# Kernel optimization log

Hardware: AMD Instinct MI355X
Metric: run time of the kernel (lower is better)

Reference implementation:

```python
import jax, jax.numpy as jnp
import numpy as np

N_NODES = 50000
N_EDGES = 800000
IN_CH = 128
HIDDEN = 32
HEADS = 4
NEG_SLOPE = 0.2


def segment_softmax(e, seg, num_segments):
    # numerically stable softmax over edges grouped by destination node
    m = jax.ops.segment_max(e, seg, num_segments=num_segments)
    ex = jnp.exp(e - m[seg])
    denom = jax.ops.segment_sum(ex, seg, num_segments=num_segments)
    return ex / denom[seg]


def gat_layer(x, src, dst, W, a_src, a_dst, b, num_nodes, concat):
    H, C = a_src.shape
    h = (x @ W).reshape(num_nodes, H, C)            # (N, H, C)
    alpha_s = jnp.einsum('nhc,hc->nh', h, a_src)    # (N, H)
    alpha_d = jnp.einsum('nhc,hc->nh', h, a_dst)    # (N, H)
    e = jax.nn.leaky_relu(alpha_s[src] + alpha_d[dst], negative_slope=NEG_SLOPE)  # (E, H)
    att = segment_softmax(e, dst, num_nodes)        # (E, H)
    out = jax.ops.segment_sum(h[src] * att[:, :, None], dst, num_segments=num_nodes)  # (N, H, C)
    if concat:
        out = out.reshape(num_nodes, H * C)
    else:
        out = out.mean(axis=1)
    return out + b


def setup_inputs() -> dict:
    key = jax.random.key(0)
    ks = jax.random.split(key, 12)
    s = 0.1
    return {
        'x': jax.random.normal(ks[0], (N_NODES, IN_CH), dtype=jnp.float32),
        'edge_index': jax.random.randint(ks[1], (2, N_EDGES), 0, N_NODES, dtype=jnp.int64),
        'W1': jax.random.normal(ks[2], (IN_CH, HEADS * HIDDEN), dtype=jnp.float32) * s,
        'a_src1': jax.random.normal(ks[3], (HEADS, HIDDEN), dtype=jnp.float32) * s,
        'a_dst1': jax.random.normal(ks[4], (HEADS, HIDDEN), dtype=jnp.float32) * s,
        'b1': jnp.zeros((HEADS * HIDDEN,), dtype=jnp.float32),
        'W2': jax.random.normal(ks[5], (HEADS * HIDDEN, 1 * HIDDEN), dtype=jnp.float32) * s,
        'a_src2': jax.random.normal(ks[6], (1, HIDDEN), dtype=jnp.float32) * s,
        'a_dst2': jax.random.normal(ks[7], (1, HIDDEN), dtype=jnp.float32) * s,
        'b2': jnp.zeros((HIDDEN,), dtype=jnp.float32),
    }


def reference(x, edge_index, W1, a_src1, a_dst1, b1, W2, a_src2, a_dst2, b2):
    n = x.shape[0]
    loops = jnp.arange(n, dtype=edge_index.dtype)
    src = jnp.concatenate([edge_index[0], loops])  # PyG GATConv add_self_loops=True
    dst = jnp.concatenate([edge_index[1], loops])
    h = gat_layer(x, src, dst, W1, a_src1, a_dst1, b1, n, concat=True)
    h = jax.nn.elu(h)  # ELU between layers (dropout=0.0)
    out = gat_layer(h, src, dst, W2, a_src2, a_dst2, b2, n, concat=False)
    return out
```

## Files before the change

kernel.cpp:

```cpp
#include <hip/hip_runtime.h>
#include <cstdint>

#define NEG_SLOPE 0.2f
#define LDA 136
#define HB  256
#define CAP 5120
#define SMEM_BYTES (64 * LDA * 2)

__device__ __forceinline__ float leaky(float v) { return v > 0.f ? v : NEG_SLOPE * v; }
__device__ __forceinline__ float elu(float v) { return v > 0.f ? v : __expf(v) - 1.f; }

typedef _Float16 half2v __attribute__((ext_vector_type(2)));
typedef _Float16 f16x8 __attribute__((ext_vector_type(8)));
typedef float f32x4 __attribute__((ext_vector_type(4)));
union H8 { float4 f4; half2v h[4]; f16x8 v8; };
union H4 { float2 f2; half2v h[2]; };
union HF2 { float2 f2; _Float16 h[4]; };
union HH { f16x8 v; half2v h[4]; };


__device__ __forceinline__ void prep_body(int bid, int G, int tid,
        const float* __restrict__ W1, const float* __restrict__ W2,
        _Float16* __restrict__ W1t, _Float16* __restrict__ W2t) {
    for (int i = bid * 256 + tid; i < 128 * 128; i += G * 256) {
        int c = i >> 7, k = i & 127;
        W1t[i] = (_Float16)W1[k * 128 + c];
    }
    for (int i = bid * 256 + tid; i < 32 * 128; i += G * 256) {
        int c = i >> 7, k = i & 127;
        W2t[i] = (_Float16)W2[k * 32 + c];
    }
}

__device__ __forceinline__ void hist_chunk(int c, int tid, int* lh,
        const int* __restrict__ dstp, int* __restrict__ hist, int E, int NB, int CH) {
    for (int t = tid; t < NB; t += 256) lh[t] = 0;
    __syncthreads();
    int e0 = c * CH, e1 = min(e0 + CH, E);
    int nv = (e1 - e0) & ~3;
    for (int i = e0 + tid * 4; i < e0 + nv; i += 1024) {
        int4 d = *(const int4*)(dstp + i);
        atomicAdd(&lh[d.x >> 8], 1);
        atomicAdd(&lh[d.y >> 8], 1);
        atomicAdd(&lh[d.z >> 8], 1);
        atomicAdd(&lh[d.w >> 8], 1);
    }
    for (int i = e0 + nv + tid; i < e1; i += 256)
        atomicAdd(&lh[dstp[i] >> 8], 1);
    __syncthreads();
    for (int t = tid; t < NB; t += 256) hist[t * HB + c] = lh[t];
}

__device__ __forceinline__ void pair_chunk(int c, int tid, int* lcur,
        const int* __restrict__ src, const int* __restrict__ dstp,
        const int* __restrict__ hist, int2* __restrict__ pairs,
        int E, int NB, int CH) {
    for (int b = tid; b < NB; b += 256) {
        const int4* row = (const int4*)(hist + b * HB);
        int s = 0;
        int c4 = c >> 2;
#pragma unroll 4
        for (int i = 0; i < c4; ++i) { int4 v = row[i]; s += v.x + v.y + v.z + v.w; }
        for (int i = c4 * 4; i < c; ++i) s += hist[b * HB + i];
        lcur[b] = s;
    }
    __syncthreads();
    int e0 = c * CH, e1 = min(e0 + CH, E);
    int nv = (e1 - e0) & ~3;
    for (int i = e0 + tid * 4; i < e0 + nv; i += 1024) {
        int4 d = *(const int4*)(dstp + i);
        int4 s = *(const int4*)(src + i);
        int b0 = d.x >> 8, b1 = d.y >> 8, b2 = d.z >> 8, b3 = d.w >> 8;
        int r0 = atomicAdd(&lcur[b0], 1);
        int r1 = atomicAdd(&lcur[b1], 1);
        int r2 = atomicAdd(&lcur[b2], 1);
        int r3 = atomicAdd(&lcur[b3], 1);
        if (r0 < CAP) pairs[(size_t)b0 * CAP + r0] = make_int2(s.x, d.x & 255);
        if (r1 < CAP) pairs[(size_t)b1 * CAP + r1] = make_int2(s.y, d.y & 255);
        if (r2 < CAP) pairs[(size_t)b2 * CAP + r2] = make_int2(s.z, d.z & 255);
        if (r3 < CAP) pairs[(size_t)b3 * CAP + r3] = make_int2(s.w, d.w & 255);
    }
    for (int i = e0 + nv + tid; i < e1; i += 256) {
        int d = dstp[i];
        int b = d >> 8;
        int r = atomicAdd(&lcur[b], 1);
        if (r < CAP) pairs[(size_t)b * CAP + r] = make_int2(src[i], d & 255);
    }
}

__device__ __forceinline__ void gemm1_tile(int b, int tid, _Float16* Ah,
        const float* __restrict__ x, const _Float16* __restrict__ W1t,
        const float* __restrict__ a_src, const float* __restrict__ a_dst,
        _Float16* __restrict__ h1h, float* __restrict__ as1, float* __restrict__ ad1,
        int n) {
    int row0 = b * 64;
    const float4* x4 = (const float4*)x;
#pragma unroll
    for (int i = 0; i < 8; ++i) {
        int idx = tid + i * 256;
        int row = idx >> 5, c4 = idx & 31;
        float4 v = make_float4(0.f, 0.f, 0.f, 0.f);
        if (row0 + row < n) v = x4[(size_t)(row0 + row) * 32 + c4];
        HF2 u;
        u.h[0] = (_Float16)v.x; u.h[1] = (_Float16)v.y;
        u.h[2] = (_Float16)v.z; u.h[3] = (_Float16)v.w;
        *(float2*)&Ah[row * LDA + c4 * 4] = u.f2;
    }
    __syncthreads();

    int l = tid & 63, w = tid >> 6;
    int lr = l & 15, lg = l >> 4;
    f16x8 af[4];
#pragma unroll
    for (int kk = 0; kk < 4; ++kk)
        af[kk] = *(const f16x8*)&Ah[(w * 16 + lr) * LDA + kk * 32 + lg * 8];
    f32x4 acc[8];
#pragma unroll
    for (int t = 0; t < 8; ++t) acc[t] = (f32x4)0.f;
#pragma unroll
    for (int t = 0; t < 8; ++t) {
#pragma unroll
        for (int kk = 0; kk < 4; ++kk) {
            f16x8 bf = *(const f16x8*)&W1t[(size_t)(t * 16 + lr) * 128 + kk * 32 + lg * 8];
            acc[t] = __builtin_amdgcn_mfma_f32_16x16x32_f16(af[kk], bf, acc[t], 0, 0, 0);
        }
    }
    __syncthreads();
#pragma unroll
    for (int t = 0; t < 8; ++t)
#pragma unroll
        for (int r = 0; r < 4; ++r)
            Ah[(w * 16 + lg * 4 + r) * LDA + t * 16 + lr] = (_Float16)acc[t][r];
    __syncthreads();
    int row = tid >> 2, q = tid & 3;
    if (row0 + row < n) {
        const float* asv = a_src + q * 32;
        const float* adv = a_dst + q * 32;
        float ps = 0.f, pd = 0.f;
#pragma unroll
        for (int j = 0; j < 4; ++j) {
            f16x8 v = *(const f16x8*)&Ah[row * LDA + q * 32 + j * 8];
            *(f16x8*)&h1h[(size_t)(row0 + row) * 128 + q * 32 + j * 8] = v;
#pragma unroll
            for (int e = 0; e < 8; ++e) {
                float f = (float)v[e];
                ps += f * asv[j * 8 + e];
                pd += f * adv[j * 8 + e];
            }
        }
        as1[(row0 + row) * 4 + q] = ps;
        ad1[(row0 + row) * 4 + q] = pd;
    }
}

__device__ __forceinline__ void csr_bucket(int b, int tid, unsigned char* smem,
        const int2* __restrict__ pairs, const int* __restrict__ hist,
        int* __restrict__ rp, int* __restrict__ col, int E, int N, int NB) {
    int* lsz    = (int*)smem;
    int* lstart = lsz + 256;
    int* lnh    = lstart + 256;
    int* lnex   = lnh + 256;
    int* lncur  = lnex + 256;
    int* wsum   = lncur + 256;
    int* woff   = wsum + 4;
    int lane = tid & 63, wv = tid >> 6;

    {
        int s = 0;
        if (tid < NB) {
            const int4* row = (const int4*)(hist + tid * HB);
#pragma unroll 8
            for (int i = 0; i < HB / 4; ++i) { int4 v = row[i]; s += v.x + v.y + v.z + v.w; }
        }
        lsz[tid] = s;
    }
    __syncthreads();
    int v = lsz[tid];
    int x = v;
#pragma unroll
    for (int o = 1; o < 64; o <<= 1) { int u = __shfl_up(x, o); if (lane >= o) x += u; }
    if (lane == 63) wsum[wv] = x;
    __syncthreads();
    if (tid == 0) { int a = 0; for (int i = 0; i < 4; ++i) { woff[i] = a; a += wsum[i]; } }
    __syncthreads();
    lstart[tid] = x - v + woff[wv];
    __syncthreads();

    if (b >= NB) { if (tid == 0) rp[N] = E; return; }
    int myStart = lstart[b];
    int S = lsz[b]; if (S > CAP) S = CAP;
    const int2* pb = pairs + (size_t)b * CAP;

    lnh[tid] = 0;
    __syncthreads();
    for (int i = tid; i < S; i += 256) atomicAdd(&lnh[pb[i].y], 1);
    __syncthreads();
    int v2 = lnh[tid];
    int x2 = v2;
#pragma unroll
    for (int o = 1; o < 64; o <<= 1) { int u = __shfl_up(x2, o); if (lane >= o) x2 += u; }
    if (lane == 63) wsum[wv] = x2;
    __syncthreads();
    if (tid == 0) { int a = 0; for (int i = 0; i < 4; ++i) { woff[i] = a; a += wsum[i]; } }
    __syncthreads();
    int ex2 = x2 - v2 + woff[wv];
    lnex[tid] = ex2;
    lncur[tid] = 0;
    int node = (b << 8) + tid;
    if (node <= N) rp[node] = myStart + ex2;
    __syncthreads();
    for (int i = tid; i < S; i += 256) {
        int2 p = pb[i];
        int r = atomicAdd(&lncur[p.y], 1);
        col[myStart + lnex[p.y] + r] = p.x;
    }
}


__global__ __launch_bounds__(256) void prep_hist_kernel(
        const float* __restrict__ W1, const float* __restrict__ W2,
        _Float16* __restrict__ W1t, _Float16* __restrict__ W2t,
        const int* __restrict__ dstp, int* __restrict__ hist, int E, int NB, int CH) {
    __shared__ int lh[256];
    int bid = (int)blockIdx.x;
    if (bid < HB) {
        hist_chunk(bid, threadIdx.x, lh, dstp, hist, E, NB, CH);
        return;
    }
    prep_body(bid - HB, (int)gridDim.x - HB, threadIdx.x, W1, W2, W1t, W2t);
}

__global__ __launch_bounds__(256) void pair_kernel(const int* __restrict__ src,
                                                   const int* __restrict__ dstp,
                                                   const int* __restrict__ hist,
                                                   int2* __restrict__ pairs,
                                                   int E, int NB, int CH) {
    __shared__ int lcur[256];
    pair_chunk(blockIdx.x, threadIdx.x, lcur, src, dstp, hist, pairs, E, NB, CH);
}

__global__ __launch_bounds__(256) void csr_gemm_kernel(
        const int2* __restrict__ pairs, const int* __restrict__ hist,
        int* __restrict__ rp, int* __restrict__ col, int E, int N, int NB, int KB,
        const float* __restrict__ x, const _Float16* __restrict__ W1t,
        const float* __restrict__ a_src, const float* __restrict__ a_dst,
        _Float16* __restrict__ h1h, float* __restrict__ as1, float* __restrict__ ad1) {
    __shared__ __align__(16) unsigned char smem[SMEM_BYTES];
    int bid = (int)blockIdx.x;
    if (bid < KB) {
        csr_bucket(bid, threadIdx.x, smem, pairs, hist, rp, col, E, N, NB);
        return;
    }
    gemm1_tile(bid - KB, threadIdx.x, (_Float16*)smem, x, W1t, a_src, a_dst,
               h1h, as1, ad1, N);
}

#define W2S 136

__global__ __launch_bounds__(256) void agg1_kernel(const _Float16* __restrict__ h1h,
                                                   const float4* __restrict__ as1,
                                                   const float4* __restrict__ ad1,
                                                   const int* __restrict__ rp,
                                                   const int* __restrict__ col,
                                                   const float* __restrict__ b1,
                                                   const _Float16* __restrict__ W2t,
                                                   const float* __restrict__ a_src2,
                                                   const float* __restrict__ a_dst2,
                                                   _Float16* __restrict__ h2h,
                                                   float* __restrict__ as2,
                                                   float* __restrict__ ad2, int n) {
    __shared__ float4 s_p[4][64];
    __shared__ _Float16 s_row[4][2][128];
    __shared__ _Float16 sW2[32 * W2S];
    int tid = threadIdx.x;
    for (int e = tid; e < 32 * 16; e += 256) {
        int c = e >> 4, k8 = e & 15;
        *(f16x8*)&sW2[c * W2S + k8 * 8] = *(const f16x8*)&W2t[c * 128 + k8 * 8];
    }
    float a2s = a_src2[tid & 31], a2d = a_dst2[tid & 31];
    __syncthreads();

    int wave = tid >> 6, lane = tid & 63;
    int h = lane >> 5, l5 = lane & 31;
    int g = l5 & 15, sub = l5 >> 4;
    int head = g >> 2;
    int nid = blockIdx.x * 8 + wave * 2 + h;
    bool vn = nid < n;
    int nc = vn ? nid : 0;
    float4* sp = s_p[wave];
    int start = rp[nc];
    int end = vn ? rp[nc + 1] : start;
    float4 adn = ad1[nc], asn = as1[nc];
    float sv = (head == 0) ? asn.x + adn.x : (head == 1) ? asn.y + adn.y
             : (head == 2) ? asn.z + adn.z : asn.w + adn.w;
    float psf_h = vn ? __expf(leaky(sv)) : 0.f;
    float dnum = 0.f;
    float4 a0 = make_float4(0.f, 0.f, 0.f, 0.f);
    float4 a1 = a0;

    for (int base = start; base < end; base += 32) {
        int i = base + l5;
        int sidx = 0;
        float4 p = make_float4(0.f, 0.f, 0.f, 0.f);
        if (i < end) {
            sidx = col[i];
            float4 a = as1[sidx];
            p.x = __expf(leaky(a.x + adn.x));
            p.y = __expf(leaky(a.y + adn.y));
            p.z = __expf(leaky(a.z + adn.z));
            p.w = __expf(leaky(a.w + adn.w));
        }
        sp[lane] = p;
        int len = min(32, end - base);
        int steps = (len + 1) >> 1;
#pragma unroll 4
        for (int s = 0; s < steps; ++s) {
            int j = s * 2 + sub;
            bool valid = j < len;
            int js = valid ? j : 0;
            int sl = (h << 5) + js;
            int rj = __shfl(sidx, sl);
            float pj = ((const float*)&sp[sl])[head];
            pj = valid ? pj : 0.f;
            H8 u = ((const H8*)(h1h + (size_t)rj * 128))[g];
            dnum += pj;
            a0.x += (float)u.h[0].x * pj; a0.y += (float)u.h[0].y * pj;
            a0.z += (float)u.h[1].x * pj; a0.w += (float)u.h[1].y * pj;
            a1.x += (float)u.h[2].x * pj; a1.y += (float)u.h[2].y * pj;
            a1.z += (float)u.h[3].x * pj; a1.w += (float)u.h[3].y * pj;
        }
    }
    if (sub == 0) {
        H8 u = ((const H8*)(h1h + (size_t)nc * 128))[g];
        dnum += psf_h;
        a0.x += (float)u.h[0].x * psf_h; a0.y += (float)u.h[0].y * psf_h;
        a0.z += (float)u.h[1].x * psf_h; a0.w += (float)u.h[1].y * psf_h;
        a1.x += (float)u.h[2].x * psf_h; a1.y += (float)u.h[2].y * psf_h;
        a1.z += (float)u.h[3].x * psf_h; a1.w += (float)u.h[3].y * psf_h;
    }
    a0.x += __shfl_xor(a0.x, 16); a0.y += __shfl_xor(a0.y, 16);
    a0.z += __shfl_xor(a0.z, 16); a0.w += __shfl_xor(a0.w, 16);
    a1.x += __shfl_xor(a1.x, 16); a1.y += __shfl_xor(a1.y, 16);
    a1.z += __shfl_xor(a1.z, 16); a1.w += __shfl_xor(a1.w, 16);
    dnum += __shfl_xor(dnum, 16);
    if (sub == 0 && vn) {
        float inv = __builtin_amdgcn_rcpf(dnum);
        const float4* b4 = (const float4*)b1;
        float4 bb0 = b4[g * 2], bb1 = b4[g * 2 + 1];
        float4 r0 = make_float4(elu(a0.x * inv + bb0.x), elu(a0.y * inv + bb0.y),
                                elu(a0.z * inv + bb0.z), elu(a0.w * inv + bb0.w));
        float4 r1 = make_float4(elu(a1.x * inv + bb1.x), elu(a1.y * inv + bb1.y),
                                elu(a1.z * inv + bb1.z), elu(a1.w * inv + bb1.w));
        H8 o8;
        o8.h[0] = half2v{(_Float16)r0.x, (_Float16)r0.y};
        o8.h[1] = half2v{(_Float16)r0.z, (_Float16)r0.w};
        o8.h[2] = half2v{(_Float16)r1.x, (_Float16)r1.y};
        o8.h[3] = half2v{(_Float16)r1.z, (_Float16)r1.w};
        *(float4*)&s_row[wave][h][g * 8] = o8.f4;
    }
    int c = l5;
    float acc2 = 0.f;
#pragma unroll
    for (int k8 = 0; k8 < 16; ++k8) {
        HH rv, wvv;
        rv.v  = *(const f16x8*)&s_row[wave][h][k8 * 8];
        wvv.v = *(const f16x8*)&sW2[c * W2S + k8 * 8];
#if __has_builtin(__builtin_amdgcn_fdot2)
        acc2 = __builtin_amdgcn_fdot2(rv.h[0], wvv.h[0], acc2, false);
        acc2 = __builtin_amdgcn_fdot2(rv.h[1], wvv.h[1], acc2, false);
        acc2 = __builtin_amdgcn_fdot2(rv.h[2], wvv.h[2], acc2, false);
        acc2 = __builtin_amdgcn_fdot2(rv.h[3], wvv.h[3], acc2, false);
#else
#pragma unroll
        for (int e = 0; e < 8; ++e) acc2 += (float)rv.v[e] * (float)wvv.v[e];
#endif
    }
    float ps = acc2 * a2s, pd = acc2 * a2d;
#pragma unroll
    for (int o = 1; o < 32; o <<= 1) { ps += __shfl_xor(ps, o); pd += __shfl_xor(pd, o); }
    if (vn) {
        h2h[(size_t)nid * 32 + c] = (_Float16)acc2;
        if (l5 == 0) { as2[nid] = ps; ad2[nid] = pd; }
    }
}

__global__ __launch_bounds__(256) void agg2_kernel(const _Float16* __restrict__ h2h,
                                                   const float* __restrict__ as2,
                                                   const float* __restrict__ ad2,
                                                   const int* __restrict__ rp,
                                                   const int* __restrict__ col,
                                                   const float* __restrict__ b2,
                                                   float* __restrict__ out, int n) {
    int wave = threadIdx.x >> 6, lane = threadIdx.x & 63;
    int h = lane >> 5, l5 = lane & 31;
    int g = l5 & 7, sub = l5 >> 3;
    int nid = blockIdx.x * 8 + wave * 2 + h;
    bool vn = nid < n;
    int nc = vn ? nid : 0;
    int start = rp[nc];
    int end = vn ? rp[nc + 1] : start;
    float adn = ad2[nc];
    float psf = vn ? __expf(leaky(as2[nc] + adn)) : 0.f;
    float dnum = 0.f;
    float4 acc = make_float4(0.f, 0.f, 0.f, 0.f);
    for (int base = start; base < end; base += 32) {
        int i = base + l5;
        int sidx = 0;
        float p = 0.f;
        if (i < end) {
            sidx = col[i];
            p = __expf(leaky(as2[sidx] + adn));
        }
        int len = min(32, end - base);
        int steps = (len + 3) >> 2;
#pragma unroll 4
        for (int s = 0; s < steps; ++s) {
            int j = s * 4 + sub;
            bool valid = j < len;
            int js = valid ? j : 0;
            int sl = (h << 5) + js;
            int rj = __shfl(sidx, sl);
            float pj = __shfl(p, sl);
            pj = valid ? pj : 0.f;
            H4 u = ((const H4*)(h2h + (size_t)rj * 32))[g];
            dnum += pj;
            acc.x += (float)u.h[0].x * pj; acc.y += (float)u.h[0].y * pj;
            acc.z += (float)u.h[1].x * pj; acc.w += (float)u.h[1].y * pj;
        }
    }
    if (sub == 0) {
        H4 u = ((const H4*)(h2h + (size_t)nc * 32))[g];
        dnum += psf;
        acc.x += (float)u.h[0].x * psf; acc.y += (float)u.h[0].y * psf;
        acc.z += (float)u.h[1].x * psf; acc.w += (float)u.h[1].y * psf;
    }
#pragma unroll
    for (int o = 8; o < 32; o <<= 1) {
        acc.x += __shfl_xor(acc.x, o); acc.y += __shfl_xor(acc.y, o);
        acc.z += __shfl_xor(acc.z, o); acc.w += __shfl_xor(acc.w, o);
        dnum += __shfl_xor(dnum, o);
    }
    if (sub == 0 && vn) {
        float inv = __builtin_amdgcn_rcpf(dnum);
        float4 bb = ((const float4*)b2)[g];
        ((float4*)(out + (size_t)nid * 32))[g] =
            make_float4(acc.x * inv + bb.x, acc.y * inv + bb.y,
                        acc.z * inv + bb.z, acc.w * inv + bb.w);
    }
}


extern "C" void kernel_launch(void* const* d_in, const int* in_sizes, int n_in,
                              void* d_out, int out_size, void* d_ws, size_t ws_size,
                              hipStream_t stream) {
    const float* x      = (const float*)d_in[0];
    const int*   ei     = (const int*)d_in[1];
    const float* W1     = (const float*)d_in[2];
    const float* a_src1 = (const float*)d_in[3];
    const float* a_dst1 = (const float*)d_in[4];
    const float* b1     = (const float*)d_in[5];
    const float* W2     = (const float*)d_in[6];
    const float* a_src2 = (const float*)d_in[7];
    const float* a_dst2 = (const float*)d_in[8];
    const float* b2     = (const float*)d_in[9];
    float* out = (float*)d_out;

    const int N = in_sizes[0] / 128;
    const int E = in_sizes[1] / 2;
    const int* src = ei;
    const int* dstp = ei + E;

    uint8_t* w = (uint8_t*)d_ws;
    auto carve = [&](size_t bytes) {
        uint8_t* p = w;
        w += (bytes + 255) & ~(size_t)255;
        return p;
    };
    _Float16* h1h = (_Float16*)carve((size_t)N * 128 * 2);
    _Float16* h2h = (_Float16*)carve((size_t)N * 32 * 2);
    _Float16* W1t = (_Float16*)carve((size_t)128 * 128 * 2);
    _Float16* W2t = (_Float16*)carve((size_t)32 * 128 * 2);
    float* as1 = (float*)carve((size_t)N * 4 * 4);
    float* ad1 = (float*)carve((size_t)N * 4 * 4);
    float* as2 = (float*)carve((size_t)N * 4);
    float* ad2 = (float*)carve((size_t)N * 4);
    int* rp    = (int*)carve((size_t)(N + 1) * 4);
    int* col   = (int*)carve((size_t)E * 4);
    int* hist  = (int*)carve((size_t)256 * HB * 4);

    const int NB = ((N - 1) >> 8) + 1;
    const int KB = (N >> 8) + 1;
    int CH = (E + HB - 1) / HB;
    CH = (CH + 3) & ~3;
    const int gemmBlocks = (N + 63) / 64;
    const int aggGroups = (N + 7) / 8;

    int2* pairs = (int2*)carve((size_t)NB * CAP * 8);

    prep_hist_kernel<<<HB + 80, 256, 0, stream>>>(W1, W2, W1t, W2t, dstp, hist, E, NB, CH);
    pair_kernel<<<HB, 256, 0, stream>>>(src, dstp, hist, pairs, E, NB, CH);
    csr_gemm_kernel<<<KB + gemmBlocks, 256, 0, stream>>>(
        pairs, hist, rp, col, E, N, NB, KB,
        x, W1t, a_src1, a_dst1, h1h, as1, ad1);
    agg1_kernel<<<aggGroups, 256, 0, stream>>>(h1h, (const float4*)as1,
                                               (const float4*)ad1, rp, col, b1,
                                               W2t, a_src2, a_dst2, h2h, as2, ad2, N);
    agg2_kernel<<<aggGroups, 256, 0, stream>>>(h2h, as2, ad2, rp, col, b2, out, N);
}
```

Before: 193.1 us.

## Fuse histogram and pair scatter into one kernel with global atomic bucket cursors

Merges the histogram and pair-scatter kernels into a single kernel. Each block counts its chunk locally, reserves a slot range per bucket with one global atomicAdd on a bucket cursor array, then scatters pairs using those offsets. The per-block histogram matrix and its prefix sums in both the pair and CSR stages go away, replacing a kernel launch with a small memset. Pair order within a bucket now depends on atomic ordering, so it is nondeterministic; the CSR stage still groups by node but column order within a node may vary.

After: 189.6 us. About the same (-1.8%).

```diff
diff --git a/kernel.cpp b/kernel.cpp
--- a/kernel.cpp
+++ b/kernel.cpp
@@ -3,7 +3,7 @@
 
 #define NEG_SLOPE 0.2f
 #define LDA 136
-#define HB  256
+#define PB  256
 #define CAP 5120
 #define SMEM_BYTES (64 * LDA * 2)
 
@@ -29,62 +29,6 @@
     for (int i = bid * 256 + tid; i < 32 * 128; i += G * 256) {
         int c = i >> 7, k = i & 127;
         W2t[i] = (_Float16)W2[k * 32 + c];
-    }
-}
-
-__device__ __forceinline__ void hist_chunk(int c, int tid, int* lh,
-        const int* __restrict__ dstp, int* __restrict__ hist, int E, int NB, int CH) {
-    for (int t = tid; t < NB; t += 256) lh[t] = 0;
-    __syncthreads();
-    int e0 = c * CH, e1 = min(e0 + CH, E);
-    int nv = (e1 - e0) & ~3;
-    for (int i = e0 + tid * 4; i < e0 + nv; i += 1024) {
-        int4 d = *(const int4*)(dstp + i);
-        atomicAdd(&lh[d.x >> 8], 1);
-        atomicAdd(&lh[d.y >> 8], 1);
-        atomicAdd(&lh[d.z >> 8], 1);
-        atomicAdd(&lh[d.w >> 8], 1);
-    }
-    for (int i = e0 + nv + tid; i < e1; i += 256)
-        atomicAdd(&lh[dstp[i] >> 8], 1);
-    __syncthreads();
-    for (int t = tid; t < NB; t += 256) hist[t * HB + c] = lh[t];
-}
-
-__device__ __forceinline__ void pair_chunk(int c, int tid, int* lcur,
-        const int* __restrict__ src, const int* __restrict__ dstp,
-        const int* __restrict__ hist, int2* __restrict__ pairs,
-        int E, int NB, int CH) {
-    for (int b = tid; b < NB; b += 256) {
-        const int4* row = (const int4*)(hist + b * HB);
-        int s = 0;
-        int c4 = c >> 2;
-#pragma unroll 4
-        for (int i = 0; i < c4; ++i) { int4 v = row[i]; s += v.x + v.y + v.z + v.w; }
-        for (int i = c4 * 4; i < c; ++i) s += hist[b * HB + i];
-        lcur[b] = s;
-    }
-    __syncthreads();
-    int e0 = c * CH, e1 = min(e0 + CH, E);
-    int nv = (e1 - e0) & ~3;
-    for (int i = e0 + tid * 4; i < e0 + nv; i += 1024) {
-        int4 d = *(const int4*)(dstp + i);
-        int4 s = *(const int4*)(src + i);
-        int b0 = d.x >> 8, b1 = d.y >> 8, b2 = d.z >> 8, b3 = d.w >> 8;
-        int r0 = atomicAdd(&lcur[b0], 1);
-        int r1 = atomicAdd(&lcur[b1], 1);
-        int r2 = atomicAdd(&lcur[b2], 1);
-        int r3 = atomicAdd(&lcur[b3], 1);
-        if (r0 < CAP) pairs[(size_t)b0 * CAP + r0] = make_int2(s.x, d.x & 255);
-        if (r1 < CAP) pairs[(size_t)b1 * CAP + r1] = make_int2(s.y, d.y & 255);
-        if (r2 < CAP) pairs[(size_t)b2 * CAP + r2] = make_int2(s.z, d.z & 255);
-        if (r3 < CAP) pairs[(size_t)b3 * CAP + r3] = make_int2(s.w, d.w & 255);
-    }
-    for (int i = e0 + nv + tid; i < e1; i += 256) {
-        int d = dstp[i];
-        int b = d >> 8;
-        int r = atomicAdd(&lcur[b], 1);
-        if (r < CAP) pairs[(size_t)b * CAP + r] = make_int2(src[i], d & 255);
     }
 }
 
@@ -153,8 +97,61 @@
     }
 }
 
+
+__global__ __launch_bounds__(256) void pairprep_kernel(
+        const int* __restrict__ src, const int* __restrict__ dstp,
+        int* __restrict__ bcur, int2* __restrict__ pairs,
+        int E, int NB, int CH,
+        const float* __restrict__ W1, const float* __restrict__ W2,
+        _Float16* __restrict__ W1t, _Float16* __restrict__ W2t) {
+    int bid = (int)blockIdx.x, tid = threadIdx.x;
+    if (bid >= PB) {
+        prep_body(bid - PB, (int)gridDim.x - PB, tid, W1, W2, W1t, W2t);
+        return;
+    }
+    __shared__ int lh[256];
+    for (int t = tid; t < NB; t += 256) lh[t] = 0;
+    __syncthreads();
+    int e0 = bid * CH, e1 = min(e0 + CH, E);
+    int nv = (e1 - e0) & ~3;
+    for (int i = e0 + tid * 4; i < e0 + nv; i += 1024) {
+        int4 d = *(const int4*)(dstp + i);
+        atomicAdd(&lh[d.x >> 8], 1);
+        atomicAdd(&lh[d.y >> 8], 1);
+        atomicAdd(&lh[d.z >> 8], 1);
+        atomicAdd(&lh[d.w >> 8], 1);
+    }
+    for (int i = e0 + nv + tid; i < e1; i += 256)
+        atomicAdd(&lh[dstp[i] >> 8], 1);
+    __syncthreads();
+    for (int t = tid; t < NB; t += 256) {
+        int c = lh[t];
+        lh[t] = (c > 0) ? atomicAdd(&bcur[t], c) : 0;
+    }
+    __syncthreads();
+    for (int i = e0 + tid * 4; i < e0 + nv; i += 1024) {
+        int4 d = *(const int4*)(dstp + i);
+        int4 s = *(const int4*)(src + i);
+        int b0 = d.x >> 8, b1 = d.y >> 8, b2 = d.z >> 8, b3 = d.w >> 8;
+        int r0 = atomicAdd(&lh[b0], 1);
+        int r1 = atomicAdd(&lh[b1], 1);
+        int r2 = atomicAdd(&lh[b2], 1);
+        int r3 = atomicAdd(&lh[b3], 1);
+        if (r0 < CAP) pairs[(size_t)b0 * CAP + r0] = make_int2(s.x, d.x & 255);
+        if (r1 < CAP) pairs[(size_t)b1 * CAP + r1] = make_int2(s.y, d.y & 255);
+        if (r2 < CAP) pairs[(size_t)b2 * CAP + r2] = make_int2(s.z, d.z & 255);
+        if (r3 < CAP) pairs[(size_t)b3 * CAP + r3] = make_int2(s.w, d.w & 255);
+    }
+    for (int i = e0 + nv + tid; i < e1; i += 256) {
+        int d = dstp[i];
+        int b = d >> 8;
+        int r = atomicAdd(&lh[b], 1);
+        if (r < CAP) pairs[(size_t)b * CAP + r] = make_int2(src[i], d & 255);
+    }
+}
+
 __device__ __forceinline__ void csr_bucket(int b, int tid, unsigned char* smem,
-        const int2* __restrict__ pairs, const int* __restrict__ hist,
+        const int2* __restrict__ pairs, const int* __restrict__ bcur,
         int* __restrict__ rp, int* __restrict__ col, int E, int N, int NB) {
     int* lsz    = (int*)smem;
     int* lstart = lsz + 256;
@@ -165,15 +162,7 @@
     int* woff   = wsum + 4;
     int lane = tid & 63, wv = tid >> 6;
 
-    {
-        int s = 0;
-        if (tid < NB) {
-            const int4* row = (const int4*)(hist + tid * HB);
-#pragma unroll 8
-            for (int i = 0; i < HB / 4; ++i) { int4 v = row[i]; s += v.x + v.y + v.z + v.w; }
-        }
-        lsz[tid] = s;
-    }
+    lsz[tid] = (tid < NB) ? bcur[tid] : 0;
     __syncthreads();
     int v = lsz[tid];
     int x = v;
@@ -216,31 +205,8 @@
     }
 }
 
-
-__global__ __launch_bounds__(256) void prep_hist_kernel(
-        const float* __restrict__ W1, const float* __restrict__ W2,
-        _Float16* __restrict__ W1t, _Float16* __restrict__ W2t,
-        const int* __restrict__ dstp, int* __restrict__ hist, int E, int NB, int CH) {
-    __shared__ int lh[256];
-    int bid = (int)blockIdx.x;
-    if (bid < HB) {
-        hist_chunk(bid, threadIdx.x, lh, dstp, hist, E, NB, CH);
-        return;
-    }
-    prep_body(bid - HB, (int)gridDim.x - HB, threadIdx.x, W1, W2, W1t, W2t);
-}
-
-__global__ __launch_bounds__(256) void pair_kernel(const int* __restrict__ src,
-                                                   const int* __restrict__ dstp,
-                                                   const int* __restrict__ hist,
-                                                   int2* __restrict__ pairs,
-                                                   int E, int NB, int CH) {
-    __shared__ int lcur[256];
-    pair_chunk(blockIdx.x, threadIdx.x, lcur, src, dstp, hist, pairs, E, NB, CH);
-}
-
 __global__ __launch_bounds__(256) void csr_gemm_kernel(
-        const int2* __restrict__ pairs, const int* __restrict__ hist,
+        const int2* __restrict__ pairs, const int* __restrict__ bcur,
         int* __restrict__ rp, int* __restrict__ col, int E, int N, int NB, int KB,
         const float* __restrict__ x, const _Float16* __restrict__ W1t,
         const float* __restrict__ a_src, const float* __restrict__ a_dst,
@@ -248,7 +214,7 @@
     __shared__ __align__(16) unsigned char smem[SMEM_BYTES];
     int bid = (int)blockIdx.x;
     if (bid < KB) {
-        csr_bucket(bid, threadIdx.x, smem, pairs, hist, rp, col, E, N, NB);
+        csr_bucket(bid, threadIdx.x, smem, pairs, bcur, rp, col, E, N, NB);
         return;
     }
     gemm1_tile(bid - KB, threadIdx.x, (_Float16*)smem, x, W1t, a_src, a_dst,
@@ -486,21 +452,22 @@
     float* ad2 = (float*)carve((size_t)N * 4);
     int* rp    = (int*)carve((size_t)(N + 1) * 4);
     int* col   = (int*)carve((size_t)E * 4);
-    int* hist  = (int*)carve((size_t)256 * HB * 4);
+    int* bcur  = (int*)carve(256 * 4);
 
     const int NB = ((N - 1) >> 8) + 1;
     const int KB = (N >> 8) + 1;
-    int CH = (E + HB - 1) / HB;
+    int CH = (E + PB - 1) / PB;
     CH = (CH + 3) & ~3;
     const int gemmBlocks = (N + 63) / 64;
     const int aggGroups = (N + 7) / 8;
 
     int2* pairs = (int2*)carve((size_t)NB * CAP * 8);
 
-    prep_hist_kernel<<<HB + 80, 256, 0, stream>>>(W1, W2, W1t, W2t, dstp, hist, E, NB, CH);
-    pair_kernel<<<HB, 256, 0, stream>>>(src, dstp, hist, pairs, E, NB, CH);
+    hipMemsetAsync(bcur, 0, 256 * 4, stream);
+    pairprep_kernel<<<PB + 80, 256, 0, stream>>>(src, dstp, bcur, pairs,
+                                                 E, NB, CH, W1, W2, W1t, W2t);
     csr_gemm_kernel<<<KB + gemmBlocks, 256, 0, stream>>>(
-        pairs, hist, rp, col, E, N, NB, KB,
+        pairs, bcur, rp, col, E, N, NB, KB,
         x, W1t, a_src1, a_dst1, h1h, as1, ad1);
     agg1_kernel<<<aggGroups, 256, 0, stream>>>(h1h, (const float4*)as1,
                                                (const float4*)ad1, rp, col, b1,
```
